# Optimization experiments

Measured on AMD Instinct MI355X. Metric: run time of the kernel, lower is better.

## Reference

```python
import jax, jax.numpy as jnp
import numpy as np

V, C, H, L, FC, OUT, WS = 512, 256, 4, 6, 1024, 192, 4
HD = C // H
B, T = 8, 1024


def setup_inputs() -> dict:
    key = jax.random.key(0)
    ks = jax.random.split(key, 24)
    d = {}
    d['emb'] = jax.random.normal(ks[0], (V, C), jnp.float32) * C ** -0.5
    d['Wq'] = jax.random.normal(ks[1], (L, C, C), jnp.float32) * 0.02
    d['Wk'] = jax.random.normal(ks[2], (L, C, C), jnp.float32) * 0.02
    d['Wv'] = jax.random.normal(ks[3], (L, C, C), jnp.float32) * 0.02
    d['Wo'] = jax.random.normal(ks[4], (L, C, C), jnp.float32) * 0.02
    d['bq'] = jnp.zeros((L, C), jnp.float32)
    d['bk'] = jnp.zeros((L, C), jnp.float32)
    d['bv'] = jnp.zeros((L, C), jnp.float32)
    d['bo'] = jnp.zeros((L, C), jnp.float32)
    d['rel_k'] = jax.random.normal(ks[5], (L, 2 * WS + 1, HD), jnp.float32) * HD ** -0.5
    d['rel_v'] = jax.random.normal(ks[6], (L, 2 * WS + 1, HD), jnp.float32) * HD ** -0.5
    d['ln1_g'] = jnp.ones((L, C), jnp.float32)
    d['ln1_b'] = jnp.zeros((L, C), jnp.float32)
    d['ln2_g'] = jnp.ones((L, C), jnp.float32)
    d['ln2_b'] = jnp.zeros((L, C), jnp.float32)
    d['ffn_w1'] = jax.random.normal(ks[7], (L, C, FC), jnp.float32) * 0.02
    d['ffn_b1'] = jnp.zeros((L, FC), jnp.float32)
    d['ffn_w2'] = jax.random.normal(ks[8], (L, FC, C), jnp.float32) * 0.02
    d['ffn_b2'] = jnp.zeros((L, C), jnp.float32)
    d['proj_w'] = jax.random.normal(ks[9], (2 * OUT, C), jnp.float32) * 0.02
    d['proj_b'] = jnp.zeros((2 * OUT,), jnp.float32)
    d['tokens'] = jax.random.randint(ks[10], (B, T), 0, V)
    d['x_lengths'] = jax.random.randint(ks[11], (B,), T // 2, T + 1)
    return d


def _rel_to_abs(x):
    # x: [B,H,L,2L-1] -> [B,H,L,L]
    b, h, l, _ = x.shape
    x = jnp.pad(x, ((0, 0), (0, 0), (0, 0), (0, 1)))
    x = x.reshape(b, h, l * 2 * l)
    x = jnp.pad(x, ((0, 0), (0, 0), (0, l - 1)))
    x = x.reshape(b, h, l + 1, 2 * l - 1)
    return x[:, :, :l, l - 1:]


def _abs_to_rel(x):
    # x: [B,H,L,L] -> [B,H,L,2L-1]
    b, h, l, _ = x.shape
    x = jnp.pad(x, ((0, 0), (0, 0), (0, 0), (0, l - 1)))
    x = x.reshape(b, h, l * (2 * l - 1))
    x = jnp.pad(x, ((0, 0), (0, 0), (l, 0)))
    x = x.reshape(b, h, l, 2 * l)
    return x[:, :, :, 1:]


def _layernorm(x, g, b):
    m = jnp.mean(x, -1, keepdims=True)
    v = jnp.var(x, -1, keepdims=True)
    return (x - m) * jax.lax.rsqrt(v + 1e-5) * g + b


def _pad_rel(emb, t):
    # [2*WS+1, HD] -> [2t-1, HD] (t > WS+1 here)
    p = t - (WS + 1)
    return jnp.pad(emb, ((p, p), (0, 0)))


def _forward(emb, Wq, Wk, Wv, Wo, bq, bk, bv, bo, rel_k, rel_v, ln1_g, ln1_b,
             ln2_g, ln2_b, ffn_w1, ffn_b1, ffn_w2, ffn_b2, proj_w, proj_b,
             tokens, x_lengths):
    b, t = tokens.shape
    x = emb[tokens] * jnp.sqrt(jnp.float32(C))          # [B,T,C]
    mask = (jnp.arange(t)[None, :] < x_lengths[:, None]).astype(x.dtype)  # [B,T]
    attn_mask = mask[:, None, None, :] * mask[:, None, :, None]           # [B,1,T,T]

    for i in range(L):
        q = (x @ Wq[i] + bq[i]).reshape(b, t, H, HD).transpose(0, 2, 1, 3)
        k = (x @ Wk[i] + bk[i]).reshape(b, t, H, HD).transpose(0, 2, 1, 3)
        v = (x @ Wv[i] + bv[i]).reshape(b, t, H, HD).transpose(0, 2, 1, 3)
        q = q * HD ** -0.5
        scores = jnp.einsum('bhqd,bhkd->bhqk', q, k)
        rk = _pad_rel(rel_k[i], t)                      # [2T-1,HD]
        scores = scores + _rel_to_abs(jnp.einsum('bhqd,md->bhqm', q, rk))
        scores = jnp.where(attn_mask > 0, scores, -1e4)
        p = jax.nn.softmax(scores, axis=-1)             # [B,H,T,T]
        o = jnp.einsum('bhqk,bhkd->bhqd', p, v)
        rv = _pad_rel(rel_v[i], t)
        o = o + jnp.einsum('bhqm,md->bhqd', _abs_to_rel(p), rv)
        o = o.transpose(0, 2, 1, 3).reshape(b, t, C) @ Wo[i] + bo[i]
        x = _layernorm(x + o, ln1_g[i], ln1_b[i])
        f = jax.nn.relu(x @ ffn_w1[i] + ffn_b1[i]) @ ffn_w2[i] + ffn_b2[i]
        x = _layernorm(x + f, ln2_g[i], ln2_b[i])
        x = x * mask[:, :, None]

    x_bct = x.transpose(0, 2, 1)                        # [B,C,T]
    stats = (jnp.einsum('oc,bct->bot', proj_w, x_bct) + proj_b[None, :, None])
    stats = stats * mask[:, None, :]
    m, logs = stats[:, :OUT], stats[:, OUT:]
    return x_bct, m, logs, mask[:, None, :]


def reference(emb, Wq, Wk, Wv, Wo, bq, bk, bv, bo, rel_k, rel_v, ln1_g, ln1_b,
              ln2_g, ln2_b, ffn_w1, ffn_b1, ffn_w2, ffn_b2, proj_w, proj_b,
              tokens, x_lengths):
    return _forward(emb, Wq, Wk, Wv, Wo, bq, bk, bv, bo, rel_k, rel_v, ln1_g,
                    ln1_b, ln2_g, ln2_b, ffn_w1, ffn_b1, ffn_w2, ffn_b2,
                    proj_w, proj_b, tokens, x_lengths)
```

## Files before the change

### kernel.cpp

```cpp
#include <hip/hip_runtime.h>

typedef unsigned short u16;
typedef __attribute__((ext_vector_type(8))) short bf16x8;
typedef __attribute__((ext_vector_type(4))) float f32x4;

#define CC   256
#define HH   4
#define HD   64
#define LL   6
#define FCD  1024
#define OUTD 192
#define WSZ  4
#define BB   8
#define TT   1024
#define BT   8192

#define OFF_XBCT 0
#define OFF_M    2097152
#define OFF_LOGS 3670016
#define OFF_MASK 5242880

#define WT_Q   0
#define WT_K   65536
#define WT_V   131072
#define WT_O   196608
#define WT_W1  262144
#define WT_W2  524288
#define WT_LAYER 786432
#define WT_TOTAL (6 * WT_LAYER)

__device__ __forceinline__ float bf2f(u16 u) {
  union { unsigned int i; float f; } v; v.i = ((unsigned int)u) << 16; return v.f;
}
__device__ __forceinline__ u16 f2bf(float f) {
  union { float f; unsigned int i; } v; v.f = f;
  unsigned int x = v.i;
  return (u16)((x + 0x7fffu + ((x >> 16) & 1u)) >> 16);
}
__device__ __forceinline__ void ldv4(const float* p, float* o) {
  float4 v = *reinterpret_cast<const float4*>(p);
  o[0] = v.x; o[1] = v.y; o[2] = v.z; o[3] = v.w;
}
__device__ __forceinline__ float ld_e(const float* p) { return *p; }
__device__ __forceinline__ float ld_e(const u16* p)   { return bf2f(*p); }
__device__ __forceinline__ void st_e(float* p, float v) { *p = v; }
__device__ __forceinline__ void st_e(u16* p, float v)   { *p = f2bf(v); }

__device__ __forceinline__ void gload16(const u16* g, u16* l) {
  __builtin_amdgcn_global_load_lds(
      (const __attribute__((address_space(1))) unsigned int*)g,
      (__attribute__((address_space(3))) unsigned int*)l, 16, 0, 0);
}

__device__ __forceinline__ void stage8(const float* p, u16* d) {
  float4 a = *reinterpret_cast<const float4*>(p);
  float4 b = *reinterpret_cast<const float4*>(p + 4);
  d[0] = f2bf(a.x); d[1] = f2bf(a.y); d[2] = f2bf(a.z); d[3] = f2bf(a.w);
  d[4] = f2bf(b.x); d[5] = f2bf(b.y); d[6] = f2bf(b.z); d[7] = f2bf(b.w);
}
__device__ __forceinline__ void stage8(const u16* p, u16* d) {
  ushort4 a = *reinterpret_cast<const ushort4*>(p);
  ushort4 b = *reinterpret_cast<const ushort4*>(p + 4);
  d[0] = a.x; d[1] = a.y; d[2] = a.z; d[3] = a.w;
  d[4] = b.x; d[5] = b.y; d[6] = b.z; d[7] = b.w;
}

__global__ __launch_bounds__(256) void tc_k(
    const float* __restrict__ W, u16* __restrict__ WT,
    int K, int N, int dstStride)
{
  __shared__ float tl[32][33];
  const int tid = threadIdx.x;
  const int lx = tid & 31;
  const int ly = tid >> 5;
  const int n0 = blockIdx.x << 5;
  const int k0 = blockIdx.y << 5;
  const int z  = blockIdx.z;
  const float* Ws = W + (size_t)z * K * N;
  u16* WTd = WT + (size_t)z * dstStride;
#pragma unroll
  for (int r = 0; r < 4; ++r)
    tl[ly + r * 8][lx] = Ws[(size_t)(k0 + ly + r * 8) * N + (n0 + lx)];
  __syncthreads();
#pragma unroll
  for (int r = 0; r < 4; ++r)
    WTd[(size_t)(n0 + ly + r * 8) * K + (k0 + lx)] = f2bf(tl[lx][ly + r * 8]);
}

__global__ __launch_bounds__(256) void embed_k(
    const float* __restrict__ emb, const int* __restrict__ tokens,
    float* __restrict__ X, u16* __restrict__ Xb)
{
  const int i = blockIdx.x * 256 + threadIdx.x;
  const int bt = i >> 6;
  const int c  = (i & 63) << 2;
  float4 e = *reinterpret_cast<const float4*>(emb + (size_t)tokens[bt] * CC + c);
  e.x *= 16.0f; e.y *= 16.0f; e.z *= 16.0f; e.w *= 16.0f;
  *reinterpret_cast<float4*>(X + (size_t)i * 4) = e;
  if (Xb)
    *reinterpret_cast<ushort4*>(Xb + (size_t)i * 4) =
        make_ushort4(f2bf(e.x), f2bf(e.y), f2bf(e.z), f2bf(e.w));
}

template <typename CT>
__global__ __launch_bounds__(256) void gemm_t_k(
    const u16* __restrict__ A, int lda, const u16* __restrict__ B, int ldb,
    const float* __restrict__ bias, CT* __restrict__ C, int ldc,
    int K, float ps, int relu, int accum)
{
  __shared__ __align__(16) u16 As[64 * 64];
  __shared__ __align__(16) u16 Bs[64 * 64];
  const int tid  = threadIdx.x;
  const int lane = tid & 63;
  const int wv   = tid >> 6;
  const int bm = blockIdx.y * 64;
  const int bn = blockIdx.x * 64;
  const int l15 = lane & 15;
  const int lq  = lane >> 4;
  const int sb0 = wv << 10;
  const int sb1 = sb0 + 512;
  const int r0  = (wv << 4) + (lane >> 3);
  const int r1  = r0 + 8;
  const int sc  = ((lane & 7) ^ (lane >> 3)) << 3;
  const int asw = (l15 & 7) << 3;

  f32x4 acc[4];
#pragma unroll
  for (int nt = 0; nt < 4; ++nt) acc[nt] = (f32x4){0.0f, 0.0f, 0.0f, 0.0f};

  for (int k0 = 0; k0 < K; k0 += 64) {
    gload16(A + (size_t)(bm + r0) * lda + (k0 + sc), As + sb0);
    gload16(A + (size_t)(bm + r1) * lda + (k0 + sc), As + sb1);
    gload16(B + (size_t)(bn + r0) * ldb + (k0 + sc), Bs + sb0);
    gload16(B + (size_t)(bn + r1) * ldb + (k0 + sc), Bs + sb1);
    __syncthreads();
#pragma unroll
    for (int s = 0; s < 2; ++s) {
      const int cbase = (s << 5) | (lq << 3);
      const bf16x8 af = *reinterpret_cast<const bf16x8*>(
          As + (((wv << 4) + l15) << 6) + (cbase ^ asw));
#pragma unroll
      for (int nt = 0; nt < 4; ++nt) {
        const bf16x8 bf = *reinterpret_cast<const bf16x8*>(
            Bs + (((nt << 4) + l15) << 6) + (cbase ^ asw));
        acc[nt] = __builtin_amdgcn_mfma_f32_16x16x32_bf16(af, bf, acc[nt], 0, 0, 0);
      }
    }
    __syncthreads();
  }

#pragma unroll
  for (int nt = 0; nt < 4; ++nt) {
#pragma unroll
    for (int r = 0; r < 4; ++r) {
      const int row = bm + (wv << 4) + (lq << 2) + r;
      const int col = bn + (nt << 4) + l15;
      float vv = acc[nt][r];
      if (bias) vv += bias[col];
      vv *= ps;
      if (relu) vv = fmaxf(vv, 0.0f);
      const size_t ci = (size_t)row * ldc + col;
      if (accum) vv += ld_e(C + ci);
      st_e(C + ci, vv);
    }
  }
}

__global__ __launch_bounds__(256) void gemm_qkv_k(
    const u16* __restrict__ Xb, const u16* __restrict__ WTl,
    const float* __restrict__ bq, const float* __restrict__ bk,
    const float* __restrict__ bv,
    u16* __restrict__ Qb, u16* __restrict__ Kb, u16* __restrict__ Vb)
{
  __shared__ __align__(16) u16 pool[2 * 64 * 64];
  u16* As = pool;
  u16* Bs = pool + 4096;
  const int tid  = threadIdx.x;
  const int lane = tid & 63;
  const int wv   = tid >> 6;
  const int bx = blockIdx.x;
  const int bm = blockIdx.y * 64;
  const int mi = bx >> 2;
  const int bnl = (bx & 3) << 6;
  const int bng = bx << 6;
  const int l15 = lane & 15;
  const int lq  = lane >> 4;
  const int sb0 = wv << 10;
  const int sb1 = sb0 + 512;
  const int r0  = (wv << 4) + (lane >> 3);
  const int r1  = r0 + 8;
  const int sc  = ((lane & 7) ^ (lane >> 3)) << 3;
  const int asw = (l15 & 7) << 3;

  const float* bias = (mi == 0) ? bq : (mi == 1) ? bk : bv;
  const float ps = (mi == 0) ? 0.125f : 1.0f;

  f32x4 acc[4];
#pragma unroll
  for (int nt = 0; nt < 4; ++nt) acc[nt] = (f32x4){0.0f, 0.0f, 0.0f, 0.0f};

  for (int k0 = 0; k0 < CC; k0 += 64) {
    gload16(Xb  + (size_t)(bm + r0) * CC + (k0 + sc), As + sb0);
    gload16(Xb  + (size_t)(bm + r1) * CC + (k0 + sc), As + sb1);
    gload16(WTl + (size_t)(bng + r0) * CC + (k0 + sc), Bs + sb0);
    gload16(WTl + (size_t)(bng + r1) * CC + (k0 + sc), Bs + sb1);
    __syncthreads();
#pragma unroll
    for (int s = 0; s < 2; ++s) {
      const int cbase = (s << 5) | (lq << 3);
      const bf16x8 af = *reinterpret_cast<const bf16x8*>(
          As + (((wv << 4) + l15) << 6) + (cbase ^ asw));
#pragma unroll
      for (int nt = 0; nt < 4; ++nt) {
        const bf16x8 bf = *reinterpret_cast<const bf16x8*>(
            Bs + (((nt << 4) + l15) << 6) + (cbase ^ asw));
        acc[nt] = __builtin_amdgcn_mfma_f32_16x16x32_bf16(af, bf, acc[nt], 0, 0, 0);
      }
    }
    __syncthreads();
  }

  if (mi != 2) {
    u16* Cp = (mi == 0) ? Qb : Kb;
#pragma unroll
    for (int nt = 0; nt < 4; ++nt) {
#pragma unroll
      for (int r = 0; r < 4; ++r) {
        const int row = bm + (wv << 4) + (lq << 2) + r;
        const int col = bnl + (nt << 4) + l15;
        Cp[(size_t)row * CC + col] = f2bf((acc[nt][r] + bias[col]) * ps);
      }
    }
  } else {
    u16* Ts = pool;
#pragma unroll
    for (int nt = 0; nt < 4; ++nt) {
#pragma unroll
      for (int r = 0; r < 4; ++r) {
        const int tl = (wv << 4) + (lq << 2) + r;
        const int dl = (nt << 4) + l15;
        Ts[dl * 72 + tl] = f2bf(acc[nt][r] + bias[bnl + dl]);
      }
    }
    __syncthreads();
    const int dl = tid >> 2;
    const size_t rowbase =
        ((size_t)((bm >> 10) * 256 + bnl + dl) << 10) + (bm & (TT - 1));
#pragma unroll
    for (int j = 0; j < 4; ++j) {
      const int c4 = ((tid & 3) << 2) + (j << 4);
      *reinterpret_cast<ushort4*>(Vb + rowbase + c4) =
          *reinterpret_cast<const ushort4*>(Ts + dl * 72 + c4);
    }
  }
}

template <typename AT, typename CT>
__global__ __launch_bounds__(256) void gemm_m_k(
    const AT* __restrict__ A, const float* __restrict__ W, int ldb,
    const float* __restrict__ bias, CT* __restrict__ C, int ldc,
    int K, float ps, int relu, int accum, int vtrans)
{
  __shared__ u16 As[64][40];
  __shared__ u16 Bs[64][40];
  const int tid  = threadIdx.x;
  const int lane = tid & 63;
  const int wv   = tid >> 6;
  const int bm = blockIdx.y * 64;
  const int bn = blockIdx.x * 64;
  const int l15 = lane & 15;
  const int lq  = lane >> 4;
  const int ar = tid >> 2;
  const int ak = (tid & 3) << 3;
  const int kr = tid & 31;
  const int nb = (tid >> 5) << 3;

  f32x4 acc[4];
#pragma unroll
  for (int nt = 0; nt < 4; ++nt) acc[nt] = (f32x4){0.0f, 0.0f, 0.0f, 0.0f};

  for (int k0 = 0; k0 < K; k0 += 32) {
    u16 t8[8];
    stage8(A + (size_t)(bm + ar) * K + (k0 + ak), t8);
    *reinterpret_cast<ushort4*>(&As[ar][ak]) =
        make_ushort4(t8[0], t8[1], t8[2], t8[3]);
    *reinterpret_cast<ushort4*>(&As[ar][ak + 4]) =
        make_ushort4(t8[4], t8[5], t8[6], t8[7]);
    float w8[8];
    ldv4(W + (size_t)(k0 + kr) * ldb + (bn + nb), w8);
    ldv4(W + (size_t)(k0 + kr) * ldb + (bn + nb + 4), w8 + 4);
#pragma unroll
    for (int j = 0; j < 8; ++j) Bs[nb + j][kr] = f2bf(w8[j]);
    __syncthreads();

    const bf16x8 af = *reinterpret_cast<const bf16x8*>(&As[(wv << 4) + l15][lq << 3]);
#pragma unroll
    for (int nt = 0; nt < 4; ++nt) {
      const bf16x8 bf = *reinterpret_cast<const bf16x8*>(&Bs[(nt << 4) + l15][lq << 3]);
      acc[nt] = __builtin_amdgcn_mfma_f32_16x16x32_bf16(af, bf, acc[nt], 0, 0, 0);
    }
    __syncthreads();
  }

#pragma unroll
  for (int nt = 0; nt < 4; ++nt) {
#pragma unroll
    for (int r = 0; r < 4; ++r) {
      const int row = bm + (wv << 4) + (lq << 2) + r;
      const int col = bn + (nt << 4) + l15;
      float vv = acc[nt][r];
      if (bias) vv += bias[col];
      vv *= ps;
      if (relu) vv = fmaxf(vv, 0.0f);
      if (vtrans) {
        const size_t dst = ((size_t)((row >> 10) * 256 + col) << 10) + (row & (TT - 1));
        st_e(C + dst, vv);
      } else {
        const size_t ci = (size_t)row * ldc + col;
        if (accum) vv += ld_e(C + ci);
        st_e(C + ci, vv);
      }
    }
  }
}

#define KLp(g) (KVpool + (g) * 4096)
#define VTp(g) (KVpool + 8192 + (g) * 4096)
__global__ __launch_bounds__(512, 4) void fattn_k(
    const u16* __restrict__ Qb, const u16* __restrict__ Kb,
    const u16* __restrict__ VbT, const float* __restrict__ rk,
    const float* __restrict__ rv, const int* __restrict__ xlen,
    u16* __restrict__ Ob)
{
  __shared__ __align__(16) u16 KVpool[4 * 64 * 64];
  __shared__ u16  Pl[2][64][64];
  __shared__ float rkl[9][64];
  __shared__ float rvl[9][68];
  __shared__ float qrel[64][12];
  __shared__ float bs_s[64][12];
  __shared__ float mrow_s[64];

  const int qt = blockIdx.x;
  const int bh = blockIdx.y;
  const int b  = bh >> 2;
  const int h  = bh & 3;
  const int tid  = threadIdx.x;
  const int lane = tid & 63;
  const int wv   = tid >> 6;
  const int grp  = wv >> 2;
  const int wvl  = wv & 3;
  const int gtid = tid & 255;
  const int l15  = lane & 15;
  const int lq   = lane >> 4;
  const int len = xlen[b];
  const int q0  = qt << 6;
  const int m0  = wvl << 4;

  if (q0 >= len) {
    for (int i = tid; i < 64 * 16; i += 512) {
      const int r = i >> 4, c4 = (i & 15) << 2;
      *reinterpret_cast<ushort4*>(
          Ob + (size_t)((b << 10) + q0 + r) * CC + (h << 6) + c4) =
          make_ushort4(0, 0, 0, 0);
    }
    return;
  }

  for (int i = tid; i < 9 * 64; i += 512) {
    rkl[i >> 6][i & 63] = rk[i];
    rvl[i >> 6][i & 63] = rv[i];
  }
  for (int i = tid; i < 64 * 16; i += 512) {
    const int r = i >> 4, c4 = (i & 15) << 2;
    *reinterpret_cast<ushort4*>(&Pl[0][r][c4]) = *reinterpret_cast<const ushort4*>(
        Qb + (size_t)((b << 10) + q0 + r) * CC + (h << 6) + c4);
  }
  for (int i = tid; i < 64 * 12; i += 512) (&bs_s[0][0])[i] = -3.0e38f;
  __syncthreads();
  for (int i = tid; i < 64 * 9; i += 512) {
    const int r = i / 9, j = i - r * 9;
    float s = 0.0f;
#pragma unroll 16
    for (int d = 0; d < 64; ++d) s += bf2f(Pl[0][r][d]) * rkl[j][d];
    qrel[r][j] = s;
  }
  __syncthreads();

  const bf16x8 qa0 = *reinterpret_cast<const bf16x8*>(&Pl[0][m0 + l15][lq << 3]);
  const bf16x8 qa1 = *reinterpret_cast<const bf16x8*>(&Pl[0][m0 + l15][32 + (lq << 3)]);

  f32x4 oacc[4];
#pragma unroll
  for (int nt = 0; nt < 4; ++nt) oacc[nt] = (f32x4){0.0f, 0.0f, 0.0f, 0.0f};
  float m_r[4] = {-3.0e38f, -3.0e38f, -3.0e38f, -3.0e38f};
  float l_r[4] = {0.0f, 0.0f, 0.0f, 0.0f};

  const int gr = gtid >> 2;
  const int gc = (gtid & 3) << 4;
  const int rswG = (gr & 7) << 3;
  const int c0w = gc ^ rswG;
  const int c1w = (gc + 8) ^ rswG;
  const int rswF = (l15 & 7) << 3;

  const int nkt = (len + 63) >> 6;
  const int nt0 = (nkt + 1) >> 1;
  const int myBeg = grp ? nt0 : 0;
  const int myEnd = grp ? nkt : nt0;

  u16* klp = KLp(grp);
  u16* vtp = VTp(grp);
  u16* plp = &Pl[grp][0][0];

  bf16x8 kp0, kp1, vq0, vq1;
  if (myBeg < myEnd) {
    const int k0 = myBeg << 6;
    const u16* p = Kb + (size_t)((b << 10) + k0 + gr) * CC + (h << 6) + gc;
    kp0 = *reinterpret_cast<const bf16x8*>(p);
    kp1 = *reinterpret_cast<const bf16x8*>(p + 8);
    const u16* pv = VbT + (size_t)((bh << 6) + gr) * TT + k0 + gc;
    vq0 = *reinterpret_cast<const bf16x8*>(pv);
    vq1 = *reinterpret_cast<const bf16x8*>(pv + 8);
  }

  for (int it = 0; it < nt0; ++it) {
    const int kt = myBeg + it;
    const bool act = (kt < myEnd);
    if (act) {
      *reinterpret_cast<bf16x8*>(klp + gr * 64 + c0w) = kp0;
      *reinterpret_cast<bf16x8*>(klp + gr * 64 + c1w) = kp1;
      *reinterpret_cast<bf16x8*>(vtp + gr * 64 + c0w) = vq0;
      *reinterpret_cast<bf16x8*>(vtp + gr * 64 + c1w) = vq1;
    }
    __syncthreads();

    if (act && kt + 1 < myEnd) {
      const int kn = (kt + 1) << 6;
      const u16* p = Kb + (size_t)((b << 10) + kn + gr) * CC + (h << 6) + gc;
      kp0 = *reinterpret_cast<const bf16x8*>(p);
      kp1 = *reinterpret_cast<const bf16x8*>(p + 8);
      const u16* pv = VbT + (size_t)((bh << 6) + gr) * TT + kn + gc;
      vq0 = *reinterpret_cast<const bf16x8*>(pv);
      vq1 = *reinterpret_cast<const bf16x8*>(pv + 8);
    }

    if (act) {
      const int k0 = kt << 6;
      f32x4 sacc[4];
#pragma unroll
      for (int nt = 0; nt < 4; ++nt) sacc[nt] = (f32x4){0.0f, 0.0f, 0.0f, 0.0f};
#pragma unroll
      for (int nt = 0; nt < 4; ++nt) {
        const int row = (nt << 4) + l15;
        const bf16x8 b0 = *reinterpret_cast<const bf16x8*>(klp + row * 64 + ((lq << 3) ^ rswF));
        const bf16x8 b1 = *reinterpret_cast<const bf16x8*>(klp + row * 64 + ((32 + (lq << 3)) ^ rswF));
        sacc[nt] = __builtin_amdgcn_mfma_f32_16x16x32_bf16(qa0, b0, sacc[nt], 0, 0, 0);
        sacc[nt] = __builtin_amdgcn_mfma_f32_16x16x32_bf16(qa1, b1, sacc[nt], 0, 0, 0);
      }
#pragma unroll
      for (int nt = 0; nt < 4; ++nt) {
#pragma unroll
        for (int reg = 0; reg < 4; ++reg) {
          const int m = m0 + (lq << 2) + reg;
          const int q = q0 + m;
          const int k = k0 + (nt << 4) + l15;
          float s = sacc[nt][reg];
          const int r = k - q;
          const bool band = (r >= -WSZ && r <= WSZ);
          if (band) s += qrel[m][r + WSZ];
          if (q >= len || k >= len) s = -10000.0f;
          if (band) bs_s[m][r + WSZ] = s;
          sacc[nt][reg] = s;
        }
      }
      float aa[4];
#pragma unroll
      for (int reg = 0; reg < 4; ++reg) {
        float mx = fmaxf(fmaxf(sacc[0][reg], sacc[1][reg]),
                         fmaxf(sacc[2][reg], sacc[3][reg]));
        mx = fmaxf(mx, __shfl_xor(mx, 1));
        mx = fmaxf(mx, __shfl_xor(mx, 2));
        mx = fmaxf(mx, __shfl_xor(mx, 4));
        mx = fmaxf(mx, __shfl_xor(mx, 8));
        const float mo = m_r[reg];
        const float mn = fmaxf(mo, mx);
        const float a = __expf(mo - mn);
        m_r[reg] = mn; aa[reg] = a; l_r[reg] *= a;
      }
#pragma unroll
      for (int reg = 0; reg < 4; ++reg) {
        const int m = m0 + (lq << 2) + reg;
        const int msw = (m & 7) << 3;
        const float mn = m_r[reg];
        float ssum = 0.0f;
#pragma unroll
        for (int nt = 0; nt < 4; ++nt) {
          const float p = __expf(sacc[nt][reg] - mn);
          ssum += p;
          plp[m * 64 + (((nt << 4) + l15) ^ msw)] = f2bf(p);
        }
        ssum += __shfl_xor(ssum, 1);
        ssum += __shfl_xor(ssum, 2);
        ssum += __shfl_xor(ssum, 4);
        ssum += __shfl_xor(ssum, 8);
        l_r[reg] += ssum;
      }
#pragma unroll
      for (int nt = 0; nt < 4; ++nt) {
#pragma unroll
        for (int reg = 0; reg < 4; ++reg) oacc[nt][reg] *= aa[reg];
      }
      {
        const int prow = m0 + l15;
        const bf16x8 p0 = *reinterpret_cast<const bf16x8*>(plp + prow * 64 + ((lq << 3) ^ rswF));
        const bf16x8 p1 = *reinterpret_cast<const bf16x8*>(plp + prow * 64 + ((32 + (lq << 3)) ^ rswF));
#pragma unroll
        for (int nt = 0; nt < 4; ++nt) {
          const int row = (nt << 4) + l15;
          const bf16x8 v0 = *reinterpret_cast<const bf16x8*>(vtp + row * 64 + ((lq << 3) ^ rswF));
          const bf16x8 v1 = *reinterpret_cast<const bf16x8*>(vtp + row * 64 + ((32 + (lq << 3)) ^ rswF));
          oacc[nt] = __builtin_amdgcn_mfma_f32_16x16x32_bf16(p0, v0, oacc[nt], 0, 0, 0);
          oacc[nt] = __builtin_amdgcn_mfma_f32_16x16x32_bf16(p1, v1, oacc[nt], 0, 0, 0);
        }
      }
    }
    __syncthreads();
  }

  float* Oc = (float*)KVpool;
  float* mxp = Oc + 64 * 68;
  float* lxp = mxp + 64;
  if (grp == 1) {
#pragma unroll
    for (int nt = 0; nt < 4; ++nt)
#pragma unroll
      for (int reg = 0; reg < 4; ++reg)
        Oc[(m0 + (lq << 2) + reg) * 68 + (nt << 4) + l15] = oacc[nt][reg];
    if (l15 == 0) {
#pragma unroll
      for (int reg = 0; reg < 4; ++reg) {
        mxp[m0 + (lq << 2) + reg] = m_r[reg];
        lxp[m0 + (lq << 2) + reg] = l_r[reg];
      }
    }
  }
  __syncthreads();
  if (grp == 0) {
    float a0c[4], a1c[4];
#pragma unroll
    for (int reg = 0; reg < 4; ++reg) {
      const int m = m0 + (lq << 2) + reg;
      const float m1 = mxp[m], l1 = lxp[m];
      const float mo = m_r[reg];
      const float mn = fmaxf(mo, m1);
      const float a0 = __expf(mo - mn);
      const float a1 = __expf(m1 - mn);
      m_r[reg] = mn;
      l_r[reg] = a0 * l_r[reg] + a1 * l1;
      a0c[reg] = a0; a1c[reg] = a1;
    }
#pragma unroll
    for (int nt = 0; nt < 4; ++nt)
#pragma unroll
      for (int reg = 0; reg < 4; ++reg) {
        const int m = m0 + (lq << 2) + reg;
        oacc[nt][reg] = a0c[reg] * oacc[nt][reg]
                      + a1c[reg] * Oc[m * 68 + (nt << 4) + l15];
      }
    if (l15 == 0) {
#pragma unroll
      for (int reg = 0; reg < 4; ++reg)
        mrow_s[m0 + (lq << 2) + reg] = m_r[reg];
    }
  }
  __syncthreads();
  for (int i = tid; i < 64 * 9; i += 512) {
    const int r = i / 9, j = i - r * 9;
    qrel[r][j] = __expf(bs_s[r][j] - mrow_s[r]);
  }
  __syncthreads();
  if (grp == 0) {
#pragma unroll
    for (int nt = 0; nt < 4; ++nt) {
#pragma unroll
      for (int reg = 0; reg < 4; ++reg) {
        const int m = m0 + (lq << 2) + reg;
        float o = oacc[nt][reg];
#pragma unroll
        for (int j = 0; j < 9; ++j) o += qrel[m][j] * rvl[j][(nt << 4) + l15];
        o *= 1.0f / l_r[reg];
        Ob[(size_t)((b << 10) + q0 + m) * CC + (h << 6) + (nt << 4) + l15] = f2bf(o);
      }
    }
  }
}

__global__ __launch_bounds__(256) void addln_k(
    float* __restrict__ X, u16* __restrict__ Xb, const float* __restrict__ R,
    const float* __restrict__ g, const float* __restrict__ be,
    const int* __restrict__ xlen, int am)
{
  const int tid = threadIdx.x;
  const int row = blockIdx.x * 4 + (tid >> 6);
  const int lane = tid & 63;
  const int b = row >> 10;
  const int t = row & (TT - 1);
  const size_t base = (size_t)row * CC + lane * 4;
  float4 xv = *reinterpret_cast<const float4*>(X + base);
  float4 rv = *reinterpret_cast<const float4*>(R + base);
  float v0 = xv.x + rv.x, v1 = xv.y + rv.y, v2 = xv.z + rv.z, v3 = xv.w + rv.w;
  float s = v0 + v1 + v2 + v3;
#pragma unroll
  for (int off = 32; off > 0; off >>= 1) s += __shfl_xor(s, off);
  const float mean = s * (1.0f / CC);
  const float d0 = v0 - mean, d1 = v1 - mean, d2 = v2 - mean, d3 = v3 - mean;
  float s2 = d0 * d0 + d1 * d1 + d2 * d2 + d3 * d3;
#pragma unroll
  for (int off = 32; off > 0; off >>= 1) s2 += __shfl_xor(s2, off);
  const float rs = rsqrtf(s2 * (1.0f / CC) + 1e-5f);
  const float4 gv = *reinterpret_cast<const float4*>(g + lane * 4);
  const float4 bv = *reinterpret_cast<const float4*>(be + lane * 4);
  float y0 = d0 * rs * gv.x + bv.x;
  float y1 = d1 * rs * gv.y + bv.y;
  float y2 = d2 * rs * gv.z + bv.z;
  float y3 = d3 * rs * gv.w + bv.w;
  if (am && t >= xlen[b]) { y0 = 0.0f; y1 = 0.0f; y2 = 0.0f; y3 = 0.0f; }
  *reinterpret_cast<float4*>(X + base) = make_float4(y0, y1, y2, y3);
  if (Xb)
    *reinterpret_cast<ushort4*>(Xb + base) =
        make_ushort4(f2bf(y0), f2bf(y1), f2bf(y2), f2bf(y3));
}

__global__ __launch_bounds__(256) void proj_k(
    const float* __restrict__ A, const float* __restrict__ W,
    const float* __restrict__ bias, const int* __restrict__ xlen,
    float* __restrict__ out)
{
  __shared__ u16 As[64][40];
  __shared__ u16 Bs[64][40];
  const int tid  = threadIdx.x;
  const int lane = tid & 63;
  const int wv   = tid >> 6;
  const int bm = blockIdx.y * 64;
  const int bn = blockIdx.x * 64;
  const int l15 = lane & 15;
  const int lq  = lane >> 4;
  const int ar = tid >> 2;
  const int ak = (tid & 3) << 3;

  f32x4 acc[4];
#pragma unroll
  for (int nt = 0; nt < 4; ++nt) acc[nt] = (f32x4){0.0f, 0.0f, 0.0f, 0.0f};

  for (int k0 = 0; k0 < CC; k0 += 32) {
    u16 t8[8];
    stage8(A + (size_t)(bm + ar) * CC + (k0 + ak), t8);
    *reinterpret_cast<ushort4*>(&As[ar][ak]) =
        make_ushort4(t8[0], t8[1], t8[2], t8[3]);
    *reinterpret_cast<ushort4*>(&As[ar][ak + 4]) =
        make_ushort4(t8[4], t8[5], t8[6], t8[7]);
    stage8(W + (size_t)(bn + ar) * CC + (k0 + ak), t8);
    *reinterpret_cast<ushort4*>(&Bs[ar][ak]) =
        make_ushort4(t8[0], t8[1], t8[2], t8[3]);
    *reinterpret_cast<ushort4*>(&Bs[ar][ak + 4]) =
        make_ushort4(t8[4], t8[5], t8[6], t8[7]);
    __syncthreads();

    const bf16x8 af = *reinterpret_cast<const bf16x8*>(&As[(wv << 4) + l15][lq << 3]);
#pragma unroll
    for (int nt = 0; nt < 4; ++nt) {
      const bf16x8 bf = *reinterpret_cast<const bf16x8*>(&Bs[(nt << 4) + l15][lq << 3]);
      acc[nt] = __builtin_amdgcn_mfma_f32_16x16x32_bf16(af, bf, acc[nt], 0, 0, 0);
    }
    __syncthreads();
  }

#pragma unroll
  for (int nt = 0; nt < 4; ++nt) {
#pragma unroll
    for (int r = 0; r < 4; ++r) {
      const int row = bm + (wv << 4) + (lq << 2) + r;
      const int bb = row >> 10;
      const int t  = row & (TT - 1);
      const int len = xlen[bb];
      const int o = bn + (nt << 4) + l15;
      float vv = acc[nt][r] + bias[o];
      if (t >= len) vv = 0.0f;
      const size_t dst = (o < OUTD)
          ? (size_t)OFF_M    + ((size_t)bb * OUTD + o) * TT + t
          : (size_t)OFF_LOGS + ((size_t)bb * OUTD + (o - OUTD)) * TT + t;
      out[dst] = vv;
    }
  }
}

__global__ __launch_bounds__(256) void pack_xbct_k(
    const float* __restrict__ X, float* __restrict__ out)
{
  const int i = blockIdx.x * 256 + threadIdx.x;
  const int b = i >> 18;
  const int c = (i >> 10) & (CC - 1);
  const int t = i & (TT - 1);
  out[OFF_XBCT + i] = X[((size_t)b << 18) + ((size_t)t << 8) + c];
}

__global__ __launch_bounds__(256) void pack_mask_k(
    const int* __restrict__ xlen, float* __restrict__ out)
{
  const int i = blockIdx.x * 256 + threadIdx.x;
  const int b = i >> 10;
  const int t = i & (TT - 1);
  out[OFF_MASK + i] = (t < xlen[b]) ? 1.0f : 0.0f;
}

extern "C" void kernel_launch(void* const* d_in, const int* in_sizes, int n_in,
                              void* d_out, int out_size, void* d_ws, size_t ws_size,
                              hipStream_t stream)
{
  (void)in_sizes; (void)n_in; (void)out_size;
  const float* emb   = (const float*)d_in[0];
  const float* Wq    = (const float*)d_in[1];
  const float* Wk    = (const float*)d_in[2];
  const float* Wv    = (const float*)d_in[3];
  const float* Wo    = (const float*)d_in[4];
  const float* bq    = (const float*)d_in[5];
  const float* bk    = (const float*)d_in[6];
  const float* bv    = (const float*)d_in[7];
  const float* bo    = (const float*)d_in[8];
  const float* relk  = (const float*)d_in[9];
  const float* relv  = (const float*)d_in[10];
  const float* ln1g  = (const float*)d_in[11];
  const float* ln1b  = (const float*)d_in[12];
  const float* ln2g  = (const float*)d_in[13];
  const float* ln2b  = (const float*)d_in[14];
  const float* W1    = (const float*)d_in[15];
  const float* b1    = (const float*)d_in[16];
  const float* W2    = (const float*)d_in[17];
  const float* b2    = (const float*)d_in[18];
  const float* projw = (const float*)d_in[19];
  const float* projb = (const float*)d_in[20];
  const int*   tokens = (const int*)d_in[21];
  const int*   xlen   = (const int*)d_in[22];
  float* out = (float*)d_out;

  const size_t TIER_B_WS = 26214400ull;
  const size_t TIER_A_WS = 38797312ull;
  const int tier = (ws_size >= TIER_A_WS) ? 0 : (ws_size >= TIER_B_WS) ? 1 : 2;

  float* X  = (float*)d_ws;
  u16* ObU = (u16*)(out + OFF_XBCT);
  u16* Kb  = (u16*)(out + OFF_M);
  u16* Vb  = (u16*)(out + OFF_LOGS);
  float* T5 = out + OFF_M;

  if (tier <= 1) {
    u16* Xb  = (u16*)(X + (size_t)BT * CC);
    u16* Wbf = Xb + (size_t)BT * CC;
    u16* pool = Wbf + WT_TOTAL;
    u16* Qb = pool;
    u16* Hc = pool;
    const int CH = (tier == 0) ? 1 : 4;
    const int Wn = FCD / CH;

    tc_k<<<dim3(8, 8, 6), 256, 0, stream>>>(Wq, Wbf + WT_Q, CC, CC, WT_LAYER);
    tc_k<<<dim3(8, 8, 6), 256, 0, stream>>>(Wk, Wbf + WT_K, CC, CC, WT_LAYER);
    tc_k<<<dim3(8, 8, 6), 256, 0, stream>>>(Wv, Wbf + WT_V, CC, CC, WT_LAYER);
    tc_k<<<dim3(8, 8, 6), 256, 0, stream>>>(Wo, Wbf + WT_O, CC, CC, WT_LAYER);
    tc_k<<<dim3(32, 8, 6), 256, 0, stream>>>(W1, Wbf + WT_W1, CC, FCD, WT_LAYER);
    tc_k<<<dim3(8, 32, 6), 256, 0, stream>>>(W2, Wbf + WT_W2, FCD, CC, WT_LAYER);

    embed_k<<<(BT * CC / 4) / 256, 256, 0, stream>>>(emb, tokens, X, Xb);

    const dim3 gQKV(12, BT / 64);
    const dim3 gC(CC / 64, BT / 64);
    const dim3 gA(16, BB * HH);
    const dim3 gP((2 * OUTD) / 64, BT / 64);

    for (int l = 0; l < LL; ++l) {
      const u16* WTl = Wbf + (size_t)l * WT_LAYER;
      gemm_qkv_k<<<gQKV, 256, 0, stream>>>(Xb, WTl, bq + (size_t)l * CC,
                                           bk + (size_t)l * CC, bv + (size_t)l * CC,
                                           Qb, Kb, Vb);
      fattn_k<<<gA, 512, 0, stream>>>(Qb, Kb, Vb,
                                      relk + (size_t)l * (2 * WSZ + 1) * HD,
                                      relv + (size_t)l * (2 * WSZ + 1) * HD, xlen, ObU);
      gemm_t_k<float><<<gC, 256, 0, stream>>>(ObU, CC, WTl + WT_O, CC,
                                              bo + (size_t)l * CC, T5, CC, CC,
                                              1.0f, 0, 0);
      addln_k<<<BT / 4, 256, 0, stream>>>(X, Xb, T5, ln1g + (size_t)l * CC,
                                          ln1b + (size_t)l * CC, xlen, 0);
      for (int c = 0; c < CH; ++c) {
        gemm_t_k<u16><<<dim3(Wn / 64, BT / 64), 256, 0, stream>>>(
            Xb, CC, WTl + WT_W1 + (size_t)c * Wn * CC, CC,
            b1 + (size_t)l * FCD + c * Wn, Hc, Wn, CC, 1.0f, 1, 0);
        gemm_t_k<float><<<gC, 256, 0, stream>>>(
            Hc, Wn, WTl + WT_W2 + (size_t)c * Wn, FCD,
            (c == 0) ? (b2 + (size_t)l * CC) : nullptr, T5, CC, Wn,
            1.0f, 0, (c > 0));
      }
      addln_k<<<BT / 4, 256, 0, stream>>>(X, Xb, T5, ln2g + (size_t)l * CC,
                                          ln2b + (size_t)l * CC, xlen, 1);
    }

    proj_k<<<gP, 256, 0, stream>>>(X, projw, projb, xlen, out);
  } else {
    u16* pool = (u16*)(X + (size_t)BT * CC);
    u16* Qb = pool;
    u16* Hc = pool;

    embed_k<<<(BT * CC / 4) / 256, 256, 0, stream>>>(emb, tokens, X, nullptr);

    const dim3 gC(CC / 64, BT / 64);
    const dim3 gA(16, BB * HH);
    const dim3 gP((2 * OUTD) / 64, BT / 64);

    for (int l = 0; l < LL; ++l) {
      const float* Wq_l = Wq + (size_t)l * CC * CC;
      const float* Wk_l = Wk + (size_t)l * CC * CC;
      const float* Wv_l = Wv + (size_t)l * CC * CC;
      const float* Wo_l = Wo + (size_t)l * CC * CC;

      gemm_m_k<float, u16><<<gC, 256, 0, stream>>>(X, Wq_l, CC, bq + (size_t)l * CC,
                                                   Qb, CC, CC, 0.125f, 0, 0, 0);
      gemm_m_k<float, u16><<<gC, 256, 0, stream>>>(X, Wk_l, CC, bk + (size_t)l * CC,
                                                   Kb, CC, CC, 1.0f, 0, 0, 0);
      gemm_m_k<float, u16><<<gC, 256, 0, stream>>>(X, Wv_l, CC, bv + (size_t)l * CC,
                                                   Vb, CC, CC, 1.0f, 0, 0, 1);
      fattn_k<<<gA, 512, 0, stream>>>(Qb, Kb, Vb,
                                      relk + (size_t)l * (2 * WSZ + 1) * HD,
                                      relv + (size_t)l * (2 * WSZ + 1) * HD, xlen, ObU);
      gemm_m_k<u16, float><<<gC, 256, 0, stream>>>(ObU, Wo_l, CC, bo + (size_t)l * CC,
                                                   T5, CC, CC, 1.0f, 0, 0, 0);
      addln_k<<<BT / 4, 256, 0, stream>>>(X, nullptr, T5, ln1g + (size_t)l * CC,
                                          ln1b + (size_t)l * CC, xlen, 0);
      for (int c = 0; c < 4; ++c) {
        gemm_m_k<float, u16><<<gC, 256, 0, stream>>>(X, W1 + (size_t)l * CC * FCD + c * 256,
                                                     FCD, b1 + (size_t)l * FCD + c * 256,
                                                     Hc, 256, CC, 1.0f, 1, 0, 0);
        gemm_m_k<u16, float><<<gC, 256, 0, stream>>>(Hc,
                                                     W2 + (size_t)l * FCD * CC + (size_t)c * 256 * CC,
                                                     CC, (c == 0) ? (b2 + (size_t)l * CC) : nullptr,
                                                     T5, CC, 256, 1.0f, 0, (c > 0), 0);
      }
      addln_k<<<BT / 4, 256, 0, stream>>>(X, nullptr, T5, ln2g + (size_t)l * CC,
                                          ln2b + (size_t)l * CC, xlen, 1);
    }

    proj_k<<<gP, 256, 0, stream>>>(X, projw, projb, xlen, out);
  }

  pack_xbct_k<<<(BB * CC * TT) / 256, 256, 0, stream>>>(X, out);
  pack_mask_k<<<(BB * TT) / 256, 256, 0, stream>>>(xlen, out);
}
```

Baseline: 776.5 us.

## Fuse output and FFN2 GEMMs with residual add and layernorm; tile xbct transpose

Adds a gemm_ln_k kernel that computes a 16-row by full-256-column GEMM tile, then adds the bias and residual and applies layernorm (with optional masking) in the epilogue, writing both fp32 and bf16 activations. This replaces the Wo GEMM plus addln pair and, in the single-chunk tier, the W2 GEMM plus addln pair. It removes the T5 intermediate round trip and two launches per layer. In exchange each block loads the full B panel for only 16 rows, which means less weight reuse and fewer waves. Separately, the final BCT transpose now goes through a padded 32x32 shared-memory tile so both reads and writes are coalesced.

```diff
diff --git a/kernel.cpp b/kernel.cpp
--- a/kernel.cpp
+++ b/kernel.cpp
@@ -162,6 +162,120 @@
       const size_t ci = (size_t)row * ldc + col;
       if (accum) vv += ld_e(C + ci);
       st_e(C + ci, vv);
+    }
+  }
+}
+
+__global__ __launch_bounds__(256) void gemm_ln_k(
+    const u16* __restrict__ A, int lda, const u16* __restrict__ B, int ldb,
+    const float* __restrict__ bias,
+    float* __restrict__ X, u16* __restrict__ Xb,
+    const float* __restrict__ g, const float* __restrict__ be,
+    const int* __restrict__ xlen, int am, int K)
+{
+  __shared__ __align__(16) u16 As[16 * 64];
+  __shared__ __align__(16) u16 Bs[256 * 64];
+  __shared__ float part[16][4];
+  __shared__ float part2[16][4];
+  const int tid  = threadIdx.x;
+  const int lane = tid & 63;
+  const int wv   = tid >> 6;
+  const int bm   = blockIdx.x << 4;
+  const int l15  = lane & 15;
+  const int lq   = lane >> 4;
+  const int sc   = ((lane & 7) ^ (lane >> 3)) << 3;
+  const int asw  = (l15 & 7) << 3;
+
+  f32x4 acc[4];
+#pragma unroll
+  for (int nt = 0; nt < 4; ++nt) acc[nt] = (f32x4){0.0f, 0.0f, 0.0f, 0.0f};
+
+  for (int k0 = 0; k0 < K; k0 += 64) {
+    if (wv < 2)
+      gload16(A + (size_t)(bm + (wv << 3) + (lane >> 3)) * lda + (k0 + sc),
+              As + (wv << 9));
+#pragma unroll
+    for (int j = 0; j < 8; ++j)
+      gload16(B + (size_t)((wv << 6) + (j << 3) + (lane >> 3)) * ldb + (k0 + sc),
+              Bs + (wv << 12) + (j << 9));
+    __syncthreads();
+#pragma unroll
+    for (int s = 0; s < 2; ++s) {
+      const int cbase = (s << 5) | (lq << 3);
+      const bf16x8 af = *reinterpret_cast<const bf16x8*>(
+          As + (l15 << 6) + (cbase ^ asw));
+#pragma unroll
+      for (int nt = 0; nt < 4; ++nt) {
+        const bf16x8 bf = *reinterpret_cast<const bf16x8*>(
+            Bs + (((wv << 6) + (nt << 4) + l15) << 6) + (cbase ^ asw));
+        acc[nt] = __builtin_amdgcn_mfma_f32_16x16x32_bf16(af, bf, acc[nt], 0, 0, 0);
+      }
+    }
+    __syncthreads();
+  }
+
+  float v[4][4];
+#pragma unroll
+  for (int nt = 0; nt < 4; ++nt) {
+    const int col = (wv << 6) + (nt << 4) + l15;
+#pragma unroll
+    for (int reg = 0; reg < 4; ++reg) {
+      const int gr = bm + (lq << 2) + reg;
+      v[nt][reg] = acc[nt][reg] + bias[col] + X[(size_t)gr * CC + col];
+    }
+  }
+  float sr[4];
+#pragma unroll
+  for (int reg = 0; reg < 4; ++reg) {
+    float s = v[0][reg] + v[1][reg] + v[2][reg] + v[3][reg];
+    s += __shfl_xor(s, 1); s += __shfl_xor(s, 2);
+    s += __shfl_xor(s, 4); s += __shfl_xor(s, 8);
+    sr[reg] = s;
+  }
+  if (l15 == 0) {
+#pragma unroll
+    for (int reg = 0; reg < 4; ++reg) part[(lq << 2) + reg][wv] = sr[reg];
+  }
+  __syncthreads();
+  float mean[4];
+#pragma unroll
+  for (int reg = 0; reg < 4; ++reg) {
+    const int r = (lq << 2) + reg;
+    mean[reg] = (part[r][0] + part[r][1] + part[r][2] + part[r][3]) * (1.0f / CC);
+  }
+#pragma unroll
+  for (int reg = 0; reg < 4; ++reg) {
+    float s2 = 0.0f;
+#pragma unroll
+    for (int nt = 0; nt < 4; ++nt) {
+      v[nt][reg] -= mean[reg];
+      s2 += v[nt][reg] * v[nt][reg];
+    }
+    s2 += __shfl_xor(s2, 1); s2 += __shfl_xor(s2, 2);
+    s2 += __shfl_xor(s2, 4); s2 += __shfl_xor(s2, 8);
+    sr[reg] = s2;
+  }
+  if (l15 == 0) {
+#pragma unroll
+    for (int reg = 0; reg < 4; ++reg) part2[(lq << 2) + reg][wv] = sr[reg];
+  }
+  __syncthreads();
+#pragma unroll
+  for (int reg = 0; reg < 4; ++reg) {
+    const int r = (lq << 2) + reg;
+    const int gr = bm + r;
+    const int b = gr >> 10;
+    const int t = gr & (TT - 1);
+    const float var = (part2[r][0] + part2[r][1] + part2[r][2] + part2[r][3]) * (1.0f / CC);
+    const float rs = rsqrtf(var + 1e-5f);
+    const bool zero = (am && t >= xlen[b]);
+#pragma unroll
+    for (int nt = 0; nt < 4; ++nt) {
+      const int col = (wv << 6) + (nt << 4) + l15;
+      float y = v[nt][reg] * rs * g[col] + be[col];
+      if (zero) y = 0.0f;
+      X[(size_t)gr * CC + col] = y;
+      Xb[(size_t)gr * CC + col] = f2bf(y);
     }
   }
 }
@@ -696,11 +810,21 @@
 __global__ __launch_bounds__(256) void pack_xbct_k(
     const float* __restrict__ X, float* __restrict__ out)
 {
-  const int i = blockIdx.x * 256 + threadIdx.x;
-  const int b = i >> 18;
-  const int c = (i >> 10) & (CC - 1);
-  const int t = i & (TT - 1);
-  out[OFF_XBCT + i] = X[((size_t)b << 18) + ((size_t)t << 8) + c];
+  __shared__ float tl[32][33];
+  const int tid = threadIdx.x;
+  const int lx = tid & 31;
+  const int ly = tid >> 5;
+  const int c0 = blockIdx.x << 5;
+  const int t0 = blockIdx.y << 5;
+  const int b  = blockIdx.z;
+#pragma unroll
+  for (int r = 0; r < 4; ++r)
+    tl[ly + r * 8][lx] = X[(((size_t)(b << 10) + t0 + ly + r * 8) << 8) + c0 + lx];
+  __syncthreads();
+#pragma unroll
+  for (int r = 0; r < 4; ++r)
+    out[OFF_XBCT + (((size_t)b * 256 + c0 + ly + r * 8) << 10) + t0 + lx] =
+        tl[lx][ly + r * 8];
 }
 
 __global__ __launch_bounds__(256) void pack_mask_k(
@@ -771,7 +895,6 @@
     embed_k<<<(BT * CC / 4) / 256, 256, 0, stream>>>(emb, tokens, X, Xb);
 
     const dim3 gQKV(12, BT / 64);
-    const dim3 gC(CC / 64, BT / 64);
     const dim3 gA(16, BB * HH);
     const dim3 gP((2 * OUTD) / 64, BT / 64);
 
@@ -783,22 +906,32 @@
       fattn_k<<<gA, 512, 0, stream>>>(Qb, Kb, Vb,
                                       relk + (size_t)l * (2 * WSZ + 1) * HD,
                                       relv + (size_t)l * (2 * WSZ + 1) * HD, xlen, ObU);
-      gemm_t_k<float><<<gC, 256, 0, stream>>>(ObU, CC, WTl + WT_O, CC,
-                                              bo + (size_t)l * CC, T5, CC, CC,
-                                              1.0f, 0, 0);
-      addln_k<<<BT / 4, 256, 0, stream>>>(X, Xb, T5, ln1g + (size_t)l * CC,
-                                          ln1b + (size_t)l * CC, xlen, 0);
-      for (int c = 0; c < CH; ++c) {
-        gemm_t_k<u16><<<dim3(Wn / 64, BT / 64), 256, 0, stream>>>(
-            Xb, CC, WTl + WT_W1 + (size_t)c * Wn * CC, CC,
-            b1 + (size_t)l * FCD + c * Wn, Hc, Wn, CC, 1.0f, 1, 0);
-        gemm_t_k<float><<<gC, 256, 0, stream>>>(
-            Hc, Wn, WTl + WT_W2 + (size_t)c * Wn, FCD,
-            (c == 0) ? (b2 + (size_t)l * CC) : nullptr, T5, CC, Wn,
-            1.0f, 0, (c > 0));
-      }
-      addln_k<<<BT / 4, 256, 0, stream>>>(X, Xb, T5, ln2g + (size_t)l * CC,
-                                          ln2b + (size_t)l * CC, xlen, 1);
+      gemm_ln_k<<<BT / 16, 256, 0, stream>>>(ObU, CC, WTl + WT_O, CC,
+                                             bo + (size_t)l * CC, X, Xb,
+                                             ln1g + (size_t)l * CC,
+                                             ln1b + (size_t)l * CC, xlen, 0, CC);
+      if (CH == 1) {
+        gemm_t_k<u16><<<dim3(FCD / 64, BT / 64), 256, 0, stream>>>(
+            Xb, CC, WTl + WT_W1, CC, b1 + (size_t)l * FCD, Hc, FCD, CC,
+            1.0f, 1, 0);
+        gemm_ln_k<<<BT / 16, 256, 0, stream>>>(Hc, FCD, WTl + WT_W2, FCD,
+                                               b2 + (size_t)l * CC, X, Xb,
+                                               ln2g + (size_t)l * CC,
+                                               ln2b + (size_t)l * CC, xlen, 1, FCD);
+      } else {
+        const dim3 gC(CC / 64, BT / 64);
+        for (int c = 0; c < CH; ++c) {
+          gemm_t_k<u16><<<dim3(Wn / 64, BT / 64), 256, 0, stream>>>(
+              Xb, CC, WTl + WT_W1 + (size_t)c * Wn * CC, CC,
+              b1 + (size_t)l * FCD + c * Wn, Hc, Wn, CC, 1.0f, 1, 0);
+          gemm_t_k<float><<<gC, 256, 0, stream>>>(
+              Hc, Wn, WTl + WT_W2 + (size_t)c * Wn, FCD,
+              (c == 0) ? (b2 + (size_t)l * CC) : nullptr, T5, CC, Wn,
+              1.0f, 0, (c > 0));
+        }
+        addln_k<<<BT / 4, 256, 0, stream>>>(X, Xb, T5, ln2g + (size_t)l * CC,
+                                            ln2b + (size_t)l * CC, xlen, 1);
+      }
     }
 
     proj_k<<<gP, 256, 0, stream>>>(X, projw, projb, xlen, out);
@@ -848,6 +981,6 @@
     proj_k<<<gP, 256, 0, stream>>>(X, projw, projb, xlen, out);
   }
 
-  pack_xbct_k<<<(BB * CC * TT) / 256, 256, 0, stream>>>(X, out);
+  pack_xbct_k<<<dim3(CC / 32, TT / 32, BB), 256, 0, stream>>>(X, out);
   pack_mask_k<<<(BB * TT) / 256, 256, 0, stream>>>(xlen, out);
 }
```

New measurement: 692.6 us. -10.8%, faster.
